# Optimization experiments

Hardware: AMD Instinct MI355X
Metric: run time of the kernel (lower is better)

The kernel has to match this reference:

```python
import jax, jax.numpy as jnp
import numpy as np

EMBED_DIM = 1024
HEAD_DIM = 64


def setup_inputs() -> dict:
    key = jax.random.key(0)
    ks = jax.random.split(key, 9)
    B, S, E, H = 4, 2048, EMBED_DIM, HEAD_DIM
    s = 1.0 / np.sqrt(E)
    return {
        "query": jax.random.normal(ks[0], (B, S, E), dtype=jnp.float32),
        "key": jax.random.normal(ks[1], (B, S, E), dtype=jnp.float32),
        "value": jax.random.normal(ks[2], (B, S, E), dtype=jnp.float32),
        "Wq": jax.random.normal(ks[3], (E, H), dtype=jnp.float32) * s,
        "bq": jnp.zeros((H,), dtype=jnp.float32),
        "Wk": jax.random.normal(ks[4], (E, H), dtype=jnp.float32) * s,
        "bk": jnp.zeros((H,), dtype=jnp.float32),
        "Wv": jax.random.normal(ks[5], (E, H), dtype=jnp.float32) * s,
        "bv": jnp.zeros((H,), dtype=jnp.float32),
    }


def reference(query, key, value, Wq, bq, Wk, bk, Wv, bv):
    # per-head linear projections: [B,S,E] @ [E,H] -> [B,S,H]
    q = jnp.einsum("bse,eh->bsh", query, Wq) + bq
    k = jnp.einsum("bse,eh->bsh", key, Wk) + bk
    v = jnp.einsum("bse,eh->bsh", value, Wv) + bv
    # NOTE: original code computes dim_k but never scales -> unscaled scores
    scores = jnp.einsum("bqh,bkh->bqk", q, k)  # [B,S,S]
    weights = jax.nn.softmax(scores, axis=-1)
    return jnp.einsum("bqk,bkh->bqh", weights, v)  # [B,S,H]
```

## Files before the change

### kernel.cpp

```cpp
#include <hip/hip_runtime.h>
#include <math.h>

#define B 4
#define S 2048
#define E 1024
#define H 64
#define BS (B*S)
#define LOG2E 1.44269504088896f
#define CINIT (-69.2493662f)

typedef float v4f __attribute__((ext_vector_type(4)));
typedef short v8s __attribute__((ext_vector_type(8)));
typedef unsigned short u16;
typedef u16 u16x8 __attribute__((ext_vector_type(8)));

#define MFMA(a,b,c) __builtin_amdgcn_mfma_f32_16x16x32_bf16(a,b,c,0,0,0)

__device__ inline u16 rh_bf16(float x){ return (u16)((__float_as_uint(x)+0x8000u)>>16); }

__global__ __launch_bounds__(256) void wsetup_kernel(
    const float* __restrict__ Wq, const float* __restrict__ Wk,
    const float* __restrict__ Wv,
    u16* __restrict__ Wt_hi, u16* __restrict__ Wt_lo)
{
    __shared__ float wt[64][65];
    const int t  = threadIdx.x;
    const int p  = blockIdx.x >> 4;
    const int e0 = (blockIdx.x & 15) * 64;
    const float* Wsrc = (p==0) ? Wq : (p==1 ? Wk : Wv);
    const float scale = (p==0) ? LOG2E : 1.0f;

    #pragma unroll
    for (int i=0;i<16;i++){
        int e_l = i*4 + (t>>6);
        wt[e_l][t&63] = Wsrc[(size_t)(e0+e_l)*H + (t&63)] * scale;
    }
    __syncthreads();

    const int h = t>>2, e16 = (t&3)*16;
    u16 hi_a[16], lo_a[16];
    #pragma unroll
    for (int j=0;j<16;j++){
        float f = wt[e16+j][h];
        unsigned u = __float_as_uint(f);
        hi_a[j] = (u16)(u>>16);
        float hif = __uint_as_float(u & 0xFFFF0000u);
        lo_a[j] = rh_bf16(f - hif);
    }
    u16* dh = Wt_hi + (size_t)(p*64+h)*E + e0 + e16;
    u16* dl = Wt_lo + (size_t)(p*64+h)*E + e0 + e16;
    *(u16x8*)dh     = *(u16x8*)&hi_a[0];
    *(u16x8*)(dh+8) = *(u16x8*)&hi_a[8];
    *(u16x8*)dl     = *(u16x8*)&lo_a[0];
    *(u16x8*)(dl+8) = *(u16x8*)&lo_a[8];
}

__global__ __launch_bounds__(128) void proj_kernel(
    const float* __restrict__ query, const float* __restrict__ key_,
    const float* __restrict__ value,
    const u16* __restrict__ Wt_hi, const u16* __restrict__ Wt_lo,
    const float* __restrict__ bq, const float* __restrict__ bk,
    const float* __restrict__ bv,
    u16* __restrict__ q_hi, u16* __restrict__ q_lo,
    u16* __restrict__ k_hi, u16* __restrict__ k_lo,
    u16* __restrict__ v_bf)
{
    __shared__ __align__(16) u16 xh[32][72], xl[32][72];
    __shared__ __align__(16) u16 wh[64][72], wl[64][72];

    const int t  = threadIdx.x;
    const int p  = blockIdx.x >> 8;
    const int r0 = (blockIdx.x & 255) * 32;
    const float* xp = (p==0) ? query : (p==1 ? key_ : value);
    const int wv = t>>6, lane = t&63, m = lane&15, quad = lane>>4;

    const int srow = t>>2, se16 = (t&3)*16;
    const int swh  = t>>1, seo  = (t&1)*32;

    v4f acc[4];
    #pragma unroll
    for (int nt=0;nt<4;nt++) acc[nt] = (v4f){0.f,0.f,0.f,0.f};

    for (int ec=0; ec<16; ec++){
        const int e0 = ec*64;
        __syncthreads();
        {
            const float* xr = xp + (size_t)(r0+srow)*E + e0 + se16;
            float4 aa[4];
            aa[0] = *(const float4*)(xr);
            aa[1] = *(const float4*)(xr+4);
            aa[2] = *(const float4*)(xr+8);
            aa[3] = *(const float4*)(xr+12);
            float fv[16];
            #pragma unroll
            for (int q4=0;q4<4;q4++){
                fv[q4*4+0]=aa[q4].x; fv[q4*4+1]=aa[q4].y;
                fv[q4*4+2]=aa[q4].z; fv[q4*4+3]=aa[q4].w;
            }
            u16 ha[16], la[16];
            #pragma unroll
            for (int j=0;j<16;j++){
                unsigned u = __float_as_uint(fv[j]);
                ha[j] = (u16)(u>>16);
                la[j] = rh_bf16(fv[j] - __uint_as_float(u & 0xFFFF0000u));
            }
            *(u16x8*)&xh[srow][se16]   = *(u16x8*)&ha[0];
            *(u16x8*)&xh[srow][se16+8] = *(u16x8*)&ha[8];
            *(u16x8*)&xl[srow][se16]   = *(u16x8*)&la[0];
            *(u16x8*)&xl[srow][se16+8] = *(u16x8*)&la[8];
        }
        {
            const u16* sh = Wt_hi + (size_t)(p*64+swh)*E + e0 + seo;
            const u16* sl = Wt_lo + (size_t)(p*64+swh)*E + e0 + seo;
            #pragma unroll
            for (int i=0;i<4;i++){
                *(u16x8*)&wh[swh][seo + i*8] = *(const u16x8*)(sh + i*8);
                *(u16x8*)&wl[swh][seo + i*8] = *(const u16x8*)(sl + i*8);
            }
        }
        __syncthreads();

        v8s ah0 = *(v8s*)&xh[wv*16+m][quad*8];
        v8s ah1 = *(v8s*)&xh[wv*16+m][32+quad*8];
        v8s al0 = *(v8s*)&xl[wv*16+m][quad*8];
        v8s al1 = *(v8s*)&xl[wv*16+m][32+quad*8];
        #pragma unroll
        for (int nt=0;nt<4;nt++){
            v8s bh0 = *(v8s*)&wh[nt*16+m][quad*8];
            v8s bh1 = *(v8s*)&wh[nt*16+m][32+quad*8];
            v8s bl0 = *(v8s*)&wl[nt*16+m][quad*8];
            v8s bl1 = *(v8s*)&wl[nt*16+m][32+quad*8];
            v4f d = acc[nt];
            d = MFMA(ah0,bh0,d); d = MFMA(ah1,bh1,d);
            d = MFMA(al0,bh0,d); d = MFMA(al1,bh1,d);
            d = MFMA(ah0,bl0,d); d = MFMA(ah1,bl1,d);
            acc[nt] = d;
        }
    }

    const float* bp = (p==0) ? bq : (p==1 ? bk : bv);
    const float bscale = (p==0) ? LOG2E : 1.0f;
    #pragma unroll
    for (int nt=0;nt<4;nt++){
        const int hl = nt*16+m;
        const float bb = bp[hl]*bscale;
        #pragma unroll
        for (int r=0;r<4;r++){
            const int gr = r0 + wv*16 + quad*4 + r;
            const float val = acc[nt][r] + bb;
            if (p<2){
                unsigned u = __float_as_uint(val);
                u16 hi = (u16)(u>>16);
                float hif = __uint_as_float(u & 0xFFFF0000u);
                u16 lo = rh_bf16(val - hif);
                u16* dh = (p==0) ? q_hi : k_hi;
                u16* dl = (p==0) ? q_lo : k_lo;
                dh[(size_t)gr*H + hl] = hi;
                dl[(size_t)gr*H + hl] = lo;
            } else {
                v_bf[(size_t)gr*H + hl] = rh_bf16(val);
            }
        }
    }
}

__global__ __launch_bounds__(256) void vtrans_kernel(
    const u16* __restrict__ v_bf, u16* __restrict__ vt)
{
    __shared__ __align__(16) u16 tl[64][72];
    const int t = threadIdx.x;
    const int b = blockIdx.x >> 5, s0 = (blockIdx.x & 31)*64;
    {
        const int r = t>>2, c16 = (t&3)*16;
        const u16* src = v_bf + (size_t)(b*S + s0 + r)*H + c16;
        *(u16x8*)&tl[r][c16]   = *(const u16x8*)src;
        *(u16x8*)&tl[r][c16+8] = *(const u16x8*)(src+8);
    }
    __syncthreads();
    const int h = t>>2, s16 = (t&3)*16;
    u16 oa[16];
    #pragma unroll
    for (int j=0;j<16;j++) oa[j] = tl[s16+j][h];
    u16* dst = vt + (size_t)(b*H + h)*S + s0 + s16;
    *(u16x8*)dst     = *(u16x8*)&oa[0];
    *(u16x8*)(dst+8) = *(u16x8*)&oa[8];
}

__global__ __launch_bounds__(256) void attn_kernel(
    const u16* __restrict__ qh_g, const u16* __restrict__ ql_g,
    const u16* __restrict__ kh_g, const u16* __restrict__ kl_g,
    const u16* __restrict__ vt_g,
    float* __restrict__ accw, float* __restrict__ lw, int ksplit)
{
    __shared__ __align__(16) u16 khe[2][16][72];
    __shared__ __align__(16) u16 kle[2][16][72];
    __shared__ __align__(16) u16 vtl[64][40];
    __shared__ __align__(16) u16 pl[4][16][40];

    const int t = threadIdx.x;
    const int wv = t>>6, lane = t&63, m = lane&15, quad = lane>>4;
    const int bid = blockIdx.x;
    const int qb = bid / ksplit, chunk = bid % ksplit;
    const int b = qb >> 5, s0 = (qb & 31)*64;
    const int ck = S / ksplit;
    const int j0base = chunk * ck;
    const int iters = ck / 32;

    const u16* qr = qh_g + (size_t)(b*S + s0 + wv*16 + m)*H + quad*8;
    const u16* qrl = ql_g + (size_t)(b*S + s0 + wv*16 + m)*H + quad*8;
    const v8s qh0 = *(const v8s*)(qr),  qh1 = *(const v8s*)(qr+32);
    const v8s ql0 = *(const v8s*)(qrl), ql1 = *(const v8s*)(qrl+32);

    v4f oacc[4];
    #pragma unroll
    for (int nt=0;nt<4;nt++) oacc[nt] = (v4f){0.f,0.f,0.f,0.f};
    float lp[4] = {0.f,0.f,0.f,0.f};
    const v4f cinit = (v4f){CINIT,CINIT,CINIT,CINIT};

    const int sj = t>>3, sh8 = (t&7)*8;
    const u16* khs = kh_g + (size_t)(b*S + j0base + sj)*H + sh8;
    const u16* kls = kl_g + (size_t)(b*S + j0base + sj)*H + sh8;
    u16* khd = &khe[sj&1][sj>>1][sh8];
    u16* kld = &kle[sj&1][sj>>1][sh8];
    const int vh = t>>2, vj8 = (t&3)*8;
    const u16* vts = vt_g + (size_t)(b*H + vh)*S + j0base + vj8;
    u16* vtd = &vtl[vh][vj8];

    for (int it=0; it<iters; ++it){
        __syncthreads();
        *(u16x8*)khd = *(const u16x8*)(khs + (size_t)it*32*H);
        *(u16x8*)kld = *(const u16x8*)(kls + (size_t)it*32*H);
        *(u16x8*)vtd = *(const u16x8*)(vts + it*32);
        __syncthreads();

        v4f sc[2];
        #pragma unroll
        for (int jt=0;jt<2;jt++){
            const u16* kr  = &khe[jt][m][quad*8];
            const u16* krl = &kle[jt][m][quad*8];
            v8s b0 = *(const v8s*)kr,  b1 = *(const v8s*)(kr+32);
            v8s c0 = *(const v8s*)krl, c1 = *(const v8s*)(krl+32);
            v4f d = cinit;
            d = MFMA(qh0,b0,d); d = MFMA(qh1,b1,d);
            d = MFMA(ql0,b0,d); d = MFMA(ql1,b1,d);
            d = MFMA(qh0,c0,d); d = MFMA(qh1,c1,d);
            sc[jt] = d;
        }

        #pragma unroll
        for (int r=0;r<4;r++){
            float p0 = exp2f(sc[0][r]);
            float p1 = exp2f(sc[1][r]);
            lp[r] += p0 + p1;
            unsigned pk = ((__float_as_uint(p0)+0x8000u)>>16)
                        | ((__float_as_uint(p1)+0x8000u) & 0xFFFF0000u);
            *(unsigned*)&pl[wv][quad*4+r][2*m] = pk;
        }
        __syncthreads();

        v8s pa = *(const v8s*)&pl[wv][m][quad*8];
        #pragma unroll
        for (int nt=0;nt<4;nt++){
            v8s vb = *(const v8s*)&vtl[nt*16+m][quad*8];
            oacc[nt] = MFMA(pa, vb, oacc[nt]);
        }
    }

    #pragma unroll
    for (int r=0;r<4;r++){
        float v = lp[r];
        v += __shfl_xor(v,1); v += __shfl_xor(v,2);
        v += __shfl_xor(v,4); v += __shfl_xor(v,8);
        lp[r] = v;
    }
    const int growb = b*S + s0 + wv*16;
    if (m==0){
        float4 lv; lv.x=lp[0]; lv.y=lp[1]; lv.z=lp[2]; lv.w=lp[3];
        *(float4*)(lw + (size_t)chunk*BS + growb + quad*4) = lv;
    }
    float* ab = accw + ((size_t)chunk*BS + growb)*H;
    #pragma unroll
    for (int nt=0;nt<4;nt++){
        #pragma unroll
        for (int r=0;r<4;r++)
            ab[(size_t)(quad*4+r)*H + nt*16 + m] = oacc[nt][r];
    }
}

__global__ __launch_bounds__(256) void merge_kernel(
    const float* __restrict__ accw, const float* __restrict__ lw,
    float* __restrict__ out, int ksplit)
{
    const int idx = blockIdx.x*256 + threadIdx.x;
    const int row = idx >> 4, h4 = (idx & 15)*4;
    float4 a = {0.f,0.f,0.f,0.f};
    float ls = 0.f;
    for (int c=0;c<ksplit;c++){
        const float4 t4 = *(const float4*)(accw + ((size_t)c*BS + row)*H + h4);
        a.x+=t4.x; a.y+=t4.y; a.z+=t4.z; a.w+=t4.w;
        ls += lw[(size_t)c*BS + row];
    }
    const float inv = __builtin_amdgcn_rcpf(ls);
    float4 o; o.x=a.x*inv; o.y=a.y*inv; o.z=a.z*inv; o.w=a.w*inv;
    *(float4*)(out + (size_t)row*H + h4) = o;
}

extern "C" void kernel_launch(void* const* d_in, const int* in_sizes, int n_in,
                              void* d_out, int out_size, void* d_ws, size_t ws_size,
                              hipStream_t stream) {
    const float* query = (const float*)d_in[0];
    const float* key_  = (const float*)d_in[1];
    const float* value = (const float*)d_in[2];
    const float* Wq    = (const float*)d_in[3];
    const float* bq    = (const float*)d_in[4];
    const float* Wk    = (const float*)d_in[5];
    const float* bk    = (const float*)d_in[6];
    const float* Wv    = (const float*)d_in[7];
    const float* bv    = (const float*)d_in[8];
    float* out = (float*)d_out;

    char* base = (char*)d_ws;
    size_t off = 0;
    u16* Wt_hi = (u16*)(base + off); off += (size_t)3*64*E*2;
    u16* Wt_lo = (u16*)(base + off); off += (size_t)3*64*E*2;
    u16* q_hi  = (u16*)(base + off); off += (size_t)BS*H*2;
    u16* q_lo  = (u16*)(base + off); off += (size_t)BS*H*2;
    u16* k_hi  = (u16*)(base + off); off += (size_t)BS*H*2;
    u16* k_lo  = (u16*)(base + off); off += (size_t)BS*H*2;
    u16* v_bf  = (u16*)(base + off); off += (size_t)BS*H*2;
    u16* vt    = (u16*)(base + off); off += (size_t)BS*H*2;
    const size_t fixed = off;
    const size_t CH = (size_t)BS*H*4 + (size_t)BS*4;

    int K = 1;
    if      (ws_size >= fixed + 8*CH) K = 8;
    else if (ws_size >= fixed + 4*CH) K = 4;
    else if (ws_size >= fixed + 2*CH) K = 2;

    float* lw   = (float*)(base + fixed);
    float* accw = (float*)(base + fixed + (size_t)K*BS*4);

    wsetup_kernel<<<48, 256, 0, stream>>>(Wq, Wk, Wv, Wt_hi, Wt_lo);
    proj_kernel<<<768, 128, 0, stream>>>(query, key_, value, Wt_hi, Wt_lo,
                                         bq, bk, bv, q_hi, q_lo, k_hi, k_lo, v_bf);
    vtrans_kernel<<<128, 256, 0, stream>>>(v_bf, vt);
    attn_kernel<<<128*K, 256, 0, stream>>>(q_hi, q_lo, k_hi, k_lo, vt, accw, lw, K);
    merge_kernel<<<512, 256, 0, stream>>>(accw, lw, out, K);
}
```

Before: 173.2 us.

## Prefetch next tiles into registers and fuse V transpose into projection

The projection and attention loops now issue the next tile's global loads into registers before the current tile is computed. The loops alternate between two register buffers, so global memory latency overlaps with MFMA work. The V transpose kernel is removed: the projection kernel writes V through an LDS tile straight into the transposed layout, which saves a launch and a global round trip. The attention loop also drops the barrier between writing and reading the per-wave P tile. This raises register pressure and assumes an even iteration count.

```diff
diff --git a/kernel.cpp b/kernel.cpp
--- a/kernel.cpp
+++ b/kernel.cpp
@@ -13,6 +13,7 @@
 typedef short v8s __attribute__((ext_vector_type(8)));
 typedef unsigned short u16;
 typedef u16 u16x8 __attribute__((ext_vector_type(8)));
+typedef u16 u16x4 __attribute__((ext_vector_type(4)));
 
 #define MFMA(a,b,c) __builtin_amdgcn_mfma_f32_16x16x32_bf16(a,b,c,0,0,0)
 
@@ -63,10 +64,11 @@
     const float* __restrict__ bv,
     u16* __restrict__ q_hi, u16* __restrict__ q_lo,
     u16* __restrict__ k_hi, u16* __restrict__ k_lo,
-    u16* __restrict__ v_bf)
+    u16* __restrict__ vt)
 {
     __shared__ __align__(16) u16 xh[32][72], xl[32][72];
     __shared__ __align__(16) u16 wh[64][72], wl[64][72];
+    __shared__ __align__(16) u16 vtile[64][40];
 
     const int t  = threadIdx.x;
     const int p  = blockIdx.x >> 8;
@@ -77,113 +79,125 @@
     const int srow = t>>2, se16 = (t&3)*16;
     const int swh  = t>>1, seo  = (t&1)*32;
 
+    const float* xb  = xp + (size_t)(r0+srow)*E + se16;
+    const u16*   shb = Wt_hi + (size_t)(p*64+swh)*E + seo;
+    const u16*   slb = Wt_lo + (size_t)(p*64+swh)*E + seo;
+
     v4f acc[4];
     #pragma unroll
     for (int nt=0;nt<4;nt++) acc[nt] = (v4f){0.f,0.f,0.f,0.f};
 
-    for (int ec=0; ec<16; ec++){
-        const int e0 = ec*64;
-        __syncthreads();
-        {
-            const float* xr = xp + (size_t)(r0+srow)*E + e0 + se16;
-            float4 aa[4];
-            aa[0] = *(const float4*)(xr);
-            aa[1] = *(const float4*)(xr+4);
-            aa[2] = *(const float4*)(xr+8);
-            aa[3] = *(const float4*)(xr+12);
-            float fv[16];
-            #pragma unroll
-            for (int q4=0;q4<4;q4++){
-                fv[q4*4+0]=aa[q4].x; fv[q4*4+1]=aa[q4].y;
-                fv[q4*4+2]=aa[q4].z; fv[q4*4+3]=aa[q4].w;
-            }
-            u16 ha[16], la[16];
-            #pragma unroll
-            for (int j=0;j<16;j++){
-                unsigned u = __float_as_uint(fv[j]);
-                ha[j] = (u16)(u>>16);
-                la[j] = rh_bf16(fv[j] - __uint_as_float(u & 0xFFFF0000u));
-            }
-            *(u16x8*)&xh[srow][se16]   = *(u16x8*)&ha[0];
-            *(u16x8*)&xh[srow][se16+8] = *(u16x8*)&ha[8];
-            *(u16x8*)&xl[srow][se16]   = *(u16x8*)&la[0];
-            *(u16x8*)&xl[srow][se16+8] = *(u16x8*)&la[8];
-        }
-        {
-            const u16* sh = Wt_hi + (size_t)(p*64+swh)*E + e0 + seo;
-            const u16* sl = Wt_lo + (size_t)(p*64+swh)*E + e0 + seo;
-            #pragma unroll
-            for (int i=0;i<4;i++){
-                *(u16x8*)&wh[swh][seo + i*8] = *(const u16x8*)(sh + i*8);
-                *(u16x8*)&wl[swh][seo + i*8] = *(const u16x8*)(sl + i*8);
-            }
-        }
-        __syncthreads();
-
-        v8s ah0 = *(v8s*)&xh[wv*16+m][quad*8];
-        v8s ah1 = *(v8s*)&xh[wv*16+m][32+quad*8];
-        v8s al0 = *(v8s*)&xl[wv*16+m][quad*8];
-        v8s al1 = *(v8s*)&xl[wv*16+m][32+quad*8];
+    float4 xA[4], xB[4];
+    u16x8  wA[8], wB[8];
+    #pragma unroll
+    for (int i=0;i<4;i++) xA[i] = *(const float4*)(xb + i*4);
+    #pragma unroll
+    for (int i=0;i<4;i++){ wA[i]   = *(const u16x8*)(shb + i*8);
+                           wA[4+i] = *(const u16x8*)(slb + i*8); }
+
+#define PROJ_ITER(EC, XC, WC, XN, WN, PREF)                                    \
+    {                                                                          \
+        __syncthreads();                                                       \
+        float fv[16] = {XC[0].x,XC[0].y,XC[0].z,XC[0].w,                       \
+                        XC[1].x,XC[1].y,XC[1].z,XC[1].w,                       \
+                        XC[2].x,XC[2].y,XC[2].z,XC[2].w,                       \
+                        XC[3].x,XC[3].y,XC[3].z,XC[3].w};                      \
+        u16 ha[16], la[16];                                                    \
+        _Pragma("unroll")                                                      \
+        for (int j=0;j<16;j++){                                                \
+            unsigned u = __float_as_uint(fv[j]);                               \
+            ha[j] = (u16)(u>>16);                                              \
+            la[j] = rh_bf16(fv[j] - __uint_as_float(u & 0xFFFF0000u));         \
+        }                                                                      \
+        *(u16x8*)&xh[srow][se16]   = *(u16x8*)&ha[0];                          \
+        *(u16x8*)&xh[srow][se16+8] = *(u16x8*)&ha[8];                          \
+        *(u16x8*)&xl[srow][se16]   = *(u16x8*)&la[0];                          \
+        *(u16x8*)&xl[srow][se16+8] = *(u16x8*)&la[8];                          \
+        *(u16x8*)&wh[swh][seo]    = WC[0];                                     \
+        *(u16x8*)&wh[swh][seo+8]  = WC[1];                                     \
+        *(u16x8*)&wh[swh][seo+16] = WC[2];                                     \
+        *(u16x8*)&wh[swh][seo+24] = WC[3];                                     \
+        *(u16x8*)&wl[swh][seo]    = WC[4];                                     \
+        *(u16x8*)&wl[swh][seo+8]  = WC[5];                                     \
+        *(u16x8*)&wl[swh][seo+16] = WC[6];                                     \
+        *(u16x8*)&wl[swh][seo+24] = WC[7];                                     \
+        if (PREF){                                                             \
+            const float* xn = xb + ((EC)+1)*64;                                \
+            XN[0] = *(const float4*)(xn);                                      \
+            XN[1] = *(const float4*)(xn+4);                                    \
+            XN[2] = *(const float4*)(xn+8);                                    \
+            XN[3] = *(const float4*)(xn+12);                                   \
+            const u16* shn = shb + ((EC)+1)*64;                                \
+            const u16* sln = slb + ((EC)+1)*64;                                \
+            WN[0]=*(const u16x8*)(shn);    WN[1]=*(const u16x8*)(shn+8);       \
+            WN[2]=*(const u16x8*)(shn+16); WN[3]=*(const u16x8*)(shn+24);      \
+            WN[4]=*(const u16x8*)(sln);    WN[5]=*(const u16x8*)(sln+8);       \
+            WN[6]=*(const u16x8*)(sln+16); WN[7]=*(const u16x8*)(sln+24);      \
+        }                                                                      \
+        __syncthreads();                                                       \
+        v8s ah0 = *(v8s*)&xh[wv*16+m][quad*8];                                 \
+        v8s ah1 = *(v8s*)&xh[wv*16+m][32+quad*8];                              \
+        v8s al0 = *(v8s*)&xl[wv*16+m][quad*8];                                 \
+        v8s al1 = *(v8s*)&xl[wv*16+m][32+quad*8];                              \
+        _Pragma("unroll")                                                      \
+        for (int nt=0;nt<4;nt++){                                              \
+            v8s bh0 = *(v8s*)&wh[nt*16+m][quad*8];                             \
+            v8s bh1 = *(v8s*)&wh[nt*16+m][32+quad*8];                          \
+            v8s bl0 = *(v8s*)&wl[nt*16+m][quad*8];                             \
+            v8s bl1 = *(v8s*)&wl[nt*16+m][32+quad*8];                          \
+            v4f d = acc[nt];                                                   \
+            d = MFMA(ah0,bh0,d); d = MFMA(ah1,bh1,d);                          \
+            d = MFMA(al0,bh0,d); d = MFMA(al1,bh1,d);                          \
+            d = MFMA(ah0,bl0,d); d = MFMA(ah1,bl1,d);                          \
+            acc[nt] = d;                                                       \
+        }                                                                      \
+    }
+
+    for (int ec2=0; ec2<16; ec2+=2){
+        PROJ_ITER(ec2,   xA, wA, xB, wB, true)
+        PROJ_ITER(ec2+1, xB, wB, xA, wA, (ec2<14))
+    }
+#undef PROJ_ITER
+
+    const float* bp = (p==0) ? bq : (p==1 ? bk : bv);
+    if (p<2){
+        const float bscale = (p==0) ? LOG2E : 1.0f;
+        u16* dh = (p==0) ? q_hi : k_hi;
+        u16* dl = (p==0) ? q_lo : k_lo;
         #pragma unroll
         for (int nt=0;nt<4;nt++){
-            v8s bh0 = *(v8s*)&wh[nt*16+m][quad*8];
-            v8s bh1 = *(v8s*)&wh[nt*16+m][32+quad*8];
-            v8s bl0 = *(v8s*)&wl[nt*16+m][quad*8];
-            v8s bl1 = *(v8s*)&wl[nt*16+m][32+quad*8];
-            v4f d = acc[nt];
-            d = MFMA(ah0,bh0,d); d = MFMA(ah1,bh1,d);
-            d = MFMA(al0,bh0,d); d = MFMA(al1,bh1,d);
-            d = MFMA(ah0,bl0,d); d = MFMA(ah1,bl1,d);
-            acc[nt] = d;
-        }
-    }
-
-    const float* bp = (p==0) ? bq : (p==1 ? bk : bv);
-    const float bscale = (p==0) ? LOG2E : 1.0f;
-    #pragma unroll
-    for (int nt=0;nt<4;nt++){
-        const int hl = nt*16+m;
-        const float bb = bp[hl]*bscale;
-        #pragma unroll
-        for (int r=0;r<4;r++){
-            const int gr = r0 + wv*16 + quad*4 + r;
-            const float val = acc[nt][r] + bb;
-            if (p<2){
+            const int hl = nt*16+m;
+            const float bb = bp[hl]*bscale;
+            #pragma unroll
+            for (int r=0;r<4;r++){
+                const int gr = r0 + wv*16 + quad*4 + r;
+                const float val = acc[nt][r] + bb;
                 unsigned u = __float_as_uint(val);
                 u16 hi = (u16)(u>>16);
                 float hif = __uint_as_float(u & 0xFFFF0000u);
                 u16 lo = rh_bf16(val - hif);
-                u16* dh = (p==0) ? q_hi : k_hi;
-                u16* dl = (p==0) ? q_lo : k_lo;
                 dh[(size_t)gr*H + hl] = hi;
                 dl[(size_t)gr*H + hl] = lo;
-            } else {
-                v_bf[(size_t)gr*H + hl] = rh_bf16(val);
             }
         }
-    }
-}
-
-__global__ __launch_bounds__(256) void vtrans_kernel(
-    const u16* __restrict__ v_bf, u16* __restrict__ vt)
-{
-    __shared__ __align__(16) u16 tl[64][72];
-    const int t = threadIdx.x;
-    const int b = blockIdx.x >> 5, s0 = (blockIdx.x & 31)*64;
-    {
-        const int r = t>>2, c16 = (t&3)*16;
-        const u16* src = v_bf + (size_t)(b*S + s0 + r)*H + c16;
-        *(u16x8*)&tl[r][c16]   = *(const u16x8*)src;
-        *(u16x8*)&tl[r][c16+8] = *(const u16x8*)(src+8);
-    }
-    __syncthreads();
-    const int h = t>>2, s16 = (t&3)*16;
-    u16 oa[16];
-    #pragma unroll
-    for (int j=0;j<16;j++) oa[j] = tl[s16+j][h];
-    u16* dst = vt + (size_t)(b*H + h)*S + s0 + s16;
-    *(u16x8*)dst     = *(u16x8*)&oa[0];
-    *(u16x8*)(dst+8) = *(u16x8*)&oa[8];
+    } else {
+        const int rlb = wv*16 + quad*4;
+        #pragma unroll
+        for (int nt=0;nt<4;nt++){
+            const int hl = nt*16+m;
+            const float bb = bp[hl];
+            u16 vv[4];
+            #pragma unroll
+            for (int r=0;r<4;r++) vv[r] = rh_bf16(acc[nt][r] + bb);
+            *(u16x4*)&vtile[hl][rlb] = *(u16x4*)&vv[0];
+        }
+        __syncthreads();
+        const int h = t>>1, so = (t&1)*16;
+        const int bidx = r0 >> 11, s0l = r0 & (S-1);
+        u16* dst = vt + ((size_t)(bidx*H + h))*S + s0l + so;
+        *(u16x8*)dst     = *(const u16x8*)&vtile[h][so];
+        *(u16x8*)(dst+8) = *(const u16x8*)&vtile[h][so+8];
+    }
 }
 
 __global__ __launch_bounds__(256) void attn_kernel(
@@ -226,45 +240,59 @@
     const u16* vts = vt_g + (size_t)(b*H + vh)*S + j0base + vj8;
     u16* vtd = &vtl[vh][vj8];
 
-    for (int it=0; it<iters; ++it){
-        __syncthreads();
-        *(u16x8*)khd = *(const u16x8*)(khs + (size_t)it*32*H);
-        *(u16x8*)kld = *(const u16x8*)(kls + (size_t)it*32*H);
-        *(u16x8*)vtd = *(const u16x8*)(vts + it*32);
-        __syncthreads();
-
-        v4f sc[2];
-        #pragma unroll
-        for (int jt=0;jt<2;jt++){
-            const u16* kr  = &khe[jt][m][quad*8];
-            const u16* krl = &kle[jt][m][quad*8];
-            v8s b0 = *(const v8s*)kr,  b1 = *(const v8s*)(kr+32);
-            v8s c0 = *(const v8s*)krl, c1 = *(const v8s*)(krl+32);
-            v4f d = cinit;
-            d = MFMA(qh0,b0,d); d = MFMA(qh1,b1,d);
-            d = MFMA(ql0,b0,d); d = MFMA(ql1,b1,d);
-            d = MFMA(qh0,c0,d); d = MFMA(qh1,c1,d);
-            sc[jt] = d;
-        }
-
-        #pragma unroll
-        for (int r=0;r<4;r++){
-            float p0 = exp2f(sc[0][r]);
-            float p1 = exp2f(sc[1][r]);
-            lp[r] += p0 + p1;
-            unsigned pk = ((__float_as_uint(p0)+0x8000u)>>16)
-                        | ((__float_as_uint(p1)+0x8000u) & 0xFFFF0000u);
-            *(unsigned*)&pl[wv][quad*4+r][2*m] = pk;
-        }
-        __syncthreads();
-
-        v8s pa = *(const v8s*)&pl[wv][m][quad*8];
-        #pragma unroll
-        for (int nt=0;nt<4;nt++){
-            v8s vb = *(const v8s*)&vtl[nt*16+m][quad*8];
-            oacc[nt] = MFMA(pa, vb, oacc[nt]);
-        }
-    }
+    u16x8 khA, klA, vtA, khB, klB, vtB;
+    khA = *(const u16x8*)khs;
+    klA = *(const u16x8*)kls;
+    vtA = *(const u16x8*)vts;
+
+#define ATTN_ITER(IT, KHC, KLC, VTC, KHN, KLN, VTN, PREF)                      \
+    {                                                                          \
+        __syncthreads();                                                       \
+        *(u16x8*)khd = KHC; *(u16x8*)kld = KLC; *(u16x8*)vtd = VTC;            \
+        if (PREF){                                                             \
+            KHN = *(const u16x8*)(khs + (size_t)((IT)+1)*32*H);                \
+            KLN = *(const u16x8*)(kls + (size_t)((IT)+1)*32*H);                \
+            VTN = *(const u16x8*)(vts + ((IT)+1)*32);                          \
+        }                                                                      \
+        __syncthreads();                                                       \
+                \
+        v4f sc[2];                                                             \
+        _Pragma("unroll")                                                      \
+        for (int jt=0;jt<2;jt++){                                              \
+            const u16* kr  = &khe[jt][m][quad*8];                              \
+            const u16* krl = &kle[jt][m][quad*8];                              \
+            v8s b0 = *(const v8s*)kr,  b1 = *(const v8s*)(kr+32);              \
+            v8s c0 = *(const v8s*)krl, c1 = *(const v8s*)(krl+32);             \
+            v4f d = cinit;                                                     \
+            d = MFMA(qh0,b0,d); d = MFMA(qh1,b1,d);                            \
+            d = MFMA(ql0,b0,d); d = MFMA(ql1,b1,d);                            \
+            d = MFMA(qh0,c0,d); d = MFMA(qh1,c1,d);                            \
+            sc[jt] = d;                                                        \
+        }                                                                      \
+            \
+        _Pragma("unroll")                                                      \
+        for (int r=0;r<4;r++){                                                 \
+            float p0 = exp2f(sc[0][r]);                     \
+            float p1 = exp2f(sc[1][r]);                     \
+            lp[r] += p0 + p1;                                                  \
+            unsigned pk = ((__float_as_uint(p0)+0x8000u)>>16)                  \
+                        | ((__float_as_uint(p1)+0x8000u) & 0xFFFF0000u);       \
+            *(unsigned*)&pl[wv][quad*4+r][2*m] = pk;                           \
+        }                                                                      \
+          \
+        v8s pa = *(const v8s*)&pl[wv][m][quad*8];                              \
+        _Pragma("unroll")                                                      \
+        for (int nt=0;nt<4;nt++){                                              \
+            v8s vb = *(const v8s*)&vtl[nt*16+m][quad*8];                       \
+            oacc[nt] = MFMA(pa, vb, oacc[nt]);                                 \
+        }                                                                      \
+    }
+
+    for (int it=0; it<iters; it+=2){
+        ATTN_ITER(it,   khA,klA,vtA, khB,klB,vtB, true)
+        ATTN_ITER(it+1, khB,klB,vtB, khA,klA,vtA, (it+2<iters))
+    }
+#undef ATTN_ITER
 
     #pragma unroll
     for (int r=0;r<4;r++){
@@ -327,7 +355,6 @@
     u16* q_lo  = (u16*)(base + off); off += (size_t)BS*H*2;
     u16* k_hi  = (u16*)(base + off); off += (size_t)BS*H*2;
     u16* k_lo  = (u16*)(base + off); off += (size_t)BS*H*2;
-    u16* v_bf  = (u16*)(base + off); off += (size_t)BS*H*2;
     u16* vt    = (u16*)(base + off); off += (size_t)BS*H*2;
     const size_t fixed = off;
     const size_t CH = (size_t)BS*H*4 + (size_t)BS*4;
@@ -342,8 +369,7 @@
 
     wsetup_kernel<<<48, 256, 0, stream>>>(Wq, Wk, Wv, Wt_hi, Wt_lo);
     proj_kernel<<<768, 128, 0, stream>>>(query, key_, value, Wt_hi, Wt_lo,
-                                         bq, bk, bv, q_hi, q_lo, k_hi, k_lo, v_bf);
-    vtrans_kernel<<<128, 256, 0, stream>>>(v_bf, vt);
+                                         bq, bk, bv, q_hi, q_lo, k_hi, k_lo, vt);
     attn_kernel<<<128*K, 256, 0, stream>>>(q_hi, q_lo, k_hi, k_lo, vt, accw, lw, K);
     merge_kernel<<<512, 256, 0, stream>>>(accw, lw, out, K);
 }
```

Result: faster. 168.2 us (-2.9%).
